# Performance work log

Measured on AMD Instinct MI355X. Metric: run time of the kernel, lower is better.

Reference implementation:

```python
import jax, jax.numpy as jnp
import numpy as np
from jax import lax

SEQ_LEN = 8192
N_FEATURES = 1
E = 128            # embedding_dim
H1 = 2 * E         # 256
H2 = 4 * E         # 512


def _lstm_params(key, in_dim, hidden):
    k1, k2, k3, k4 = jax.random.split(key, 4)
    s = 1.0 / np.sqrt(hidden)
    return (
        jax.random.uniform(k1, (4 * hidden, in_dim), jnp.float32, -s, s),   # Wih
        jax.random.uniform(k2, (4 * hidden, hidden), jnp.float32, -s, s),   # Whh
        jax.random.uniform(k3, (4 * hidden,), jnp.float32, -s, s),          # bih
        jax.random.uniform(k4, (4 * hidden,), jnp.float32, -s, s),          # bhh
    )


def lstm(x, Wih, Whh, bih, bhh):
    """Single-layer PyTorch-convention LSTM over x:[T,in]. Returns (ys:[T,H], h_T:[H])."""
    H = Whh.shape[1]
    # precompute input contribution for all timesteps (memory-bound GEMM once)
    xg = x @ Wih.T + (bih + bhh)  # [T, 4H]

    def step(carry, gx):
        h, c = carry
        g = gx + h @ Whh.T
        i, f, gc, o = jnp.split(g, 4)
        i = jax.nn.sigmoid(i)
        f = jax.nn.sigmoid(f)
        gc = jnp.tanh(gc)
        o = jax.nn.sigmoid(o)
        c = f * c + i * gc
        h = o * jnp.tanh(c)
        return (h, c), h

    init = (jnp.zeros((H,), x.dtype), jnp.zeros((H,), x.dtype))
    (hT, _), ys = lax.scan(step, init, xg)
    return ys, hT


def setup_inputs() -> dict:
    key = jax.random.key(0)
    keys = jax.random.split(key, 8)
    inp = {"x": jax.random.normal(keys[0], (SEQ_LEN, N_FEATURES), jnp.float32)}
    # encoder: n_features -> H2 -> H1 -> E
    for name, k, din, dh in [("e1", keys[1], N_FEATURES, H2), ("e2", keys[2], H2, H1), ("e3", keys[3], H1, E),
                             ("d1", keys[4], E, E), ("d2", keys[5], E, H1), ("d3", keys[6], H1, H2)]:
        Wih, Whh, bih, bhh = _lstm_params(k, din, dh)
        inp[name + "_Wih"], inp[name + "_Whh"], inp[name + "_bih"], inp[name + "_bhh"] = Wih, Whh, bih, bhh
    ko1, ko2 = jax.random.split(keys[7])
    s = 1.0 / np.sqrt(H2)
    inp["out_W"] = jax.random.uniform(ko1, (N_FEATURES, H2), jnp.float32, -s, s)
    inp["out_b"] = jax.random.uniform(ko2, (N_FEATURES,), jnp.float32, -s, s)
    return inp


def reference(x,
              e1_Wih, e1_Whh, e1_bih, e1_bhh,
              e2_Wih, e2_Whh, e2_bih, e2_bhh,
              e3_Wih, e3_Whh, e3_bih, e3_bhh,
              d1_Wih, d1_Whh, d1_bih, d1_bhh,
              d2_Wih, d2_Whh, d2_bih, d2_bhh,
              d3_Wih, d3_Whh, d3_bih, d3_bhh,
              out_W, out_b):
    # --- encoder ---
    xs = x.reshape(SEQ_LEN, N_FEATURES)
    ys, _ = lstm(xs, e1_Wih, e1_Whh, e1_bih, e1_bhh)   # [T, H2]
    ys, _ = lstm(ys, e2_Wih, e2_Whh, e2_bih, e2_bhh)   # [T, H1]
    _, hT = lstm(ys, e3_Wih, e3_Whh, e3_bih, e3_bhh)   # hT: [E]
    z = hT.reshape(N_FEATURES, E)                       # [1, E]
    # --- decoder: repeat latent across time ---
    zr = jnp.tile(z.reshape(1, E), (SEQ_LEN, 1))        # [T, E]
    ys, _ = lstm(zr, d1_Wih, d1_Whh, d1_bih, d1_bhh)    # [T, E]
    ys, _ = lstm(ys, d2_Wih, d2_Whh, d2_bih, d2_bhh)    # [T, H1]
    ys, _ = lstm(ys, d3_Wih, d3_Whh, d3_bih, d3_bhh)    # [T, H2]
    return ys @ out_W.T + out_b                          # [T, 1]
```

## Files before the change

kernel.cpp:

```cpp
#include <hip/hip_runtime.h>
#include <stdint.h>

#define T_LEN 8192

__device__ __forceinline__ float sigf(float x) {
    return 1.0f / (1.0f + __expf(-x));
}
__device__ __forceinline__ float tanh_fast(float x) {
    float e = __expf(2.0f * x);
    return 1.0f - 2.0f / (e + 1.0f);
}

template<int H, int NWG, int TPB, int SUBS, int XGMODE, int LID, bool WRITE_YS, bool WRITE_Z>
__global__ __launch_bounds__(TPB, TPB / 256)
void lstm_scan(const float* __restrict__ Whh,
               const float* __restrict__ xg,
               const float* __restrict__ wih0,
               const float* __restrict__ bih,
               const float* __restrict__ bhh,
               float* __restrict__ ys,
               unsigned long long* __restrict__ hst,
               float* __restrict__ zout)
{
    constexpr int ROWS = 4 * H / NWG;
    constexpr int HJ   = H / NWG;
    constexpr int CH   = H / SUBS;
    constexpr int CHP  = CH + 4;
    static_assert(ROWS * SUBS == TPB, "bad layout");
    static_assert(4 * SUBS <= 64, "gate group must fit a wave");

    const int tid = threadIdx.x;
    const int wg  = (NWG > 1) ? blockIdx.x : 0;
    const int q   = tid / SUBS;
    const int sub = tid % SUBS;
    const int jj  = q >> 2;
    const int g   = q & 3;
    const int grow = g * H + wg * HJ + jj;

    __shared__ float hbuf[2 * SUBS * CHP];
    __shared__ float xsh[XGMODE == 1 ? T_LEN : 1];
    __shared__ int abortf;

    float4 wreg[CH / 4];
    {
        const float4* wr = (const float4*)(Whh + (size_t)grow * H + sub * CH);
        #pragma unroll
        for (int i = 0; i < CH / 4; ++i) wreg[i] = wr[i];
    }

    float w0 = 0.f, bs = 0.f, xgc = 0.f;
    if constexpr (XGMODE == 1) { w0 = wih0[grow]; bs = bih[grow] + bhh[grow]; }
    if constexpr (XGMODE == 2) { xgc = xg[grow]; }
    if constexpr (XGMODE == 1) {
        for (int k = tid; k < T_LEN; k += TPB) xsh[k] = xg[k];
    }

    for (int k = tid; k < 2 * SUBS * CHP; k += TPB) hbuf[k] = 0.f;
    if (tid == 0) abortf = 0;

    const bool writer = (tid % (4 * SUBS)) == 0;
    const int  wjj    = tid / (4 * SUBS);
    float c = 0.f;

    float xgv = 0.f;
    if constexpr (XGMODE == 0) { if (sub == 0) xgv = xg[grow]; }

    for (int t = 0; t < T_LEN; ++t) {
        float xgn = 0.f;
        if constexpr (XGMODE == 0) {
            if (sub == 0 && t + 1 < T_LEN) xgn = xg[(size_t)(t + 1) * (4 * H) + grow];
        }

        if constexpr (NWG > 1) {
            if (t > 0 && tid < H && (tid / HJ) != wg) {
                const size_t idx = (size_t)(t - 1) * H + tid;
                const unsigned want = (unsigned)(LID * T_LEN + t);
                unsigned long long v;
                int spin = 0;
                for (;;) {
                    v = __hip_atomic_load(&hst[idx], __ATOMIC_RELAXED,
                                          __HIP_MEMORY_SCOPE_AGENT);
                    if ((unsigned)(v >> 32) == want) break;
                    if (++spin >= (1 << 22)) { abortf = 1; break; }
                }
                union { unsigned u; float f; } cv;
                cv.u = (unsigned)v;
                hbuf[(t & 1) * SUBS * CHP + (tid / CH) * CHP + (tid % CH)] = cv.f;
            }
        }
        __syncthreads();
        if constexpr (NWG > 1) { if (abortf) break; }

        const float* hb = &hbuf[(t & 1) * SUBS * CHP + sub * CHP];
        float4 a4 = make_float4(0.f, 0.f, 0.f, 0.f);
        #pragma unroll
        for (int i = 0; i < CH / 4; ++i) {
            float4 hv = *(const float4*)&hb[i * 4];
            float4 wv = wreg[i];
            a4.x = fmaf(wv.x, hv.x, a4.x);
            a4.y = fmaf(wv.y, hv.y, a4.y);
            a4.z = fmaf(wv.z, hv.z, a4.z);
            a4.w = fmaf(wv.w, hv.w, a4.w);
        }
        float acc = (a4.x + a4.y) + (a4.z + a4.w);
        #pragma unroll
        for (int d = 1; d < SUBS; d <<= 1) acc += __shfl_xor(acc, d);

        float base;
        if constexpr (XGMODE == 0)      base = xgv;
        else if constexpr (XGMODE == 1) base = fmaf(xsh[t], w0, bs);
        else                            base = xgc;
        float gv = acc + base;
        float av = (g == 2) ? tanh_fast(gv) : sigf(gv);

        float fv = __shfl_down(av, SUBS);
        float gc = __shfl_down(av, 2 * SUBS);
        float ov = __shfl_down(av, 3 * SUBS);

        if (writer) {
            c = fmaf(fv, c, av * gc);
            float h = ov * tanh_fast(c);
            const int e = wg * HJ + wjj;
            hbuf[((t + 1) & 1) * SUBS * CHP + (e / CH) * CHP + (e % CH)] = h;
            if constexpr (WRITE_YS) ys[(size_t)t * H + e] = h;
            if constexpr (NWG > 1) {
                union { float f; unsigned u; } cv;
                cv.f = h;
                unsigned long long pk =
                    ((unsigned long long)(unsigned)(LID * T_LEN + t + 1) << 32) | cv.u;
                __hip_atomic_store(&hst[(size_t)t * H + e], pk,
                                   __ATOMIC_RELAXED, __HIP_MEMORY_SCOPE_AGENT);
            }
            if constexpr (WRITE_Z) { if (t == T_LEN - 1) zout[e] = h; }
        }
        if constexpr (XGMODE == 0) xgv = xgn;
    }
}

__global__ __launch_bounds__(256)
void gemm_bias(const float* __restrict__ A, const float* __restrict__ B,
               const float* __restrict__ bih, const float* __restrict__ bhh,
               float* __restrict__ C, int M, int N, int K)
{
    __shared__ float As[16][72];
    __shared__ float Bs[16][72];
    const int tid = threadIdx.x;
    const int bm = blockIdx.y * 64;
    const int bn = blockIdx.x * 64;
    const int tm = (tid / 16) * 4;
    const int tn = (tid % 16) * 4;
    const int lr = tid >> 2;
    const int lc = (tid & 3) * 4;
    float acc[4][4] = {{0.f}};
    for (int k0 = 0; k0 < K; k0 += 16) {
        float4 va = *(const float4*)&A[(size_t)(bm + lr) * K + k0 + lc];
        float4 vb = *(const float4*)&B[(size_t)(bn + lr) * K + k0 + lc];
        As[lc + 0][lr] = va.x; As[lc + 1][lr] = va.y;
        As[lc + 2][lr] = va.z; As[lc + 3][lr] = va.w;
        Bs[lc + 0][lr] = vb.x; Bs[lc + 1][lr] = vb.y;
        Bs[lc + 2][lr] = vb.z; Bs[lc + 3][lr] = vb.w;
        __syncthreads();
        #pragma unroll
        for (int kk = 0; kk < 16; ++kk) {
            float4 av = *(const float4*)&As[kk][tm];
            float4 bv = *(const float4*)&Bs[kk][tn];
            float ar[4] = {av.x, av.y, av.z, av.w};
            float br[4] = {bv.x, bv.y, bv.z, bv.w};
            #pragma unroll
            for (int i = 0; i < 4; ++i)
                #pragma unroll
                for (int j = 0; j < 4; ++j)
                    acc[i][j] = fmaf(ar[i], br[j], acc[i][j]);
        }
        __syncthreads();
    }
    float bsum[4];
    #pragma unroll
    for (int j = 0; j < 4; ++j) bsum[j] = bih[bn + tn + j] + bhh[bn + tn + j];
    #pragma unroll
    for (int i = 0; i < 4; ++i) {
        float4 o;
        o.x = acc[i][0] + bsum[0];
        o.y = acc[i][1] + bsum[1];
        o.z = acc[i][2] + bsum[2];
        o.w = acc[i][3] + bsum[3];
        *(float4*)&C[(size_t)(bm + tm + i) * N + bn + tn] = o;
    }
}

__global__ __launch_bounds__(512)
void xg_const_d1(const float* __restrict__ z, const float* __restrict__ Wih,
                 const float* __restrict__ bih, const float* __restrict__ bhh,
                 float* __restrict__ xgd1)
{
    __shared__ float zs[128];
    const int tid = threadIdx.x;
    if (tid < 128) zs[tid] = z[tid];
    __syncthreads();
    const float4* wr = (const float4*)(Wih + (size_t)tid * 128);
    float4 a4 = make_float4(0.f, 0.f, 0.f, 0.f);
    #pragma unroll
    for (int i = 0; i < 32; ++i) {
        float4 w = wr[i];
        float4 h = *(const float4*)&zs[i * 4];
        a4.x = fmaf(w.x, h.x, a4.x); a4.y = fmaf(w.y, h.y, a4.y);
        a4.z = fmaf(w.z, h.z, a4.z); a4.w = fmaf(w.w, h.w, a4.w);
    }
    xgd1[tid] = (a4.x + a4.y) + (a4.z + a4.w) + bih[tid] + bhh[tid];
}

__global__ __launch_bounds__(256)
void out_gemv(const float* __restrict__ ys, const float* __restrict__ Wo,
              const float* __restrict__ bo, float* __restrict__ out)
{
    const int lane = threadIdx.x & 63;
    const int wid  = threadIdx.x >> 6;
    const int t = blockIdx.x * 4 + wid;
    const float* row = ys + (size_t)t * 512;
    float a = 0.f;
    #pragma unroll
    for (int i = 0; i < 8; ++i) a = fmaf(row[lane + i * 64], Wo[lane + i * 64], a);
    #pragma unroll
    for (int d = 1; d < 64; d <<= 1) a += __shfl_xor(a, d);
    if (lane == 0) out[t] = a + bo[0];
}

template<int H, int NWG, int TPB, int SUBS, int XGMODE, int LID, bool YS, bool Z>
static void launch_scan(const float* whh, const float* xg, const float* wih0,
                        const float* bih, const float* bhh, float* ys,
                        unsigned long long* hst, float* zout, hipStream_t stream)
{
    auto kfn = lstm_scan<H, NWG, TPB, SUBS, XGMODE, LID, YS, Z>;
    if (NWG > 1) {
        void* args[8] = {&whh, &xg, &wih0, &bih, &bhh, &ys, &hst, &zout};
        hipError_t e = hipLaunchCooperativeKernel(reinterpret_cast<void*>(kfn),
                                                  dim3(NWG), dim3(TPB), args, 0u, stream);
        if (e == hipSuccess) return;
    }
    kfn<<<dim3(NWG), dim3(TPB), 0, stream>>>(whh, xg, wih0, bih, bhh, ys, hst, zout);
}

extern "C" void kernel_launch(void* const* d_in, const int* in_sizes, int n_in,
                              void* d_out, int out_size, void* d_ws, size_t ws_size,
                              hipStream_t stream)
{
    (void)in_sizes; (void)n_in; (void)out_size;
    const float* x = (const float*)d_in[0];
    const float* Wih[6]; const float* Whh[6]; const float* Bih[6]; const float* Bhh[6];
    for (int l = 0; l < 6; ++l) {
        Wih[l] = (const float*)d_in[1 + l * 4 + 0];
        Whh[l] = (const float*)d_in[1 + l * 4 + 1];
        Bih[l] = (const float*)d_in[1 + l * 4 + 2];
        Bhh[l] = (const float*)d_in[1 + l * 4 + 3];
    }
    const float* outW = (const float*)d_in[25];
    const float* outb = (const float*)d_in[26];

    char* ws = (char*)d_ws;
    float* XG  = (float*)(ws);
    float* ysA = (float*)(ws + ((size_t)64 << 20));
    float* ysB = (float*)(ws + ((size_t)80 << 20));
    unsigned long long* HST = (unsigned long long*)(ws + ((size_t)96 << 20));
    float* z    = (float*)(ws + ((size_t)128 << 20));
    float* xgd1 = (float*)(ws + ((size_t)128 << 20) + 1024);
    if (ws_size < (((size_t)128 << 20) + 4096)) return;

    launch_scan<512, 32, 512, 8, 1, 1, true, false>(Whh[0], x, Wih[0], Bih[0], Bhh[0],
                                                    ysA, HST, nullptr, stream);
    gemm_bias<<<dim3(1024 / 64, T_LEN / 64), 256, 0, stream>>>(ysA, Wih[1], Bih[1], Bhh[1],
                                                               XG, T_LEN, 1024, 512);
    launch_scan<256, 16, 512, 8, 0, 2, true, false>(Whh[1], XG, nullptr, nullptr, nullptr,
                                                    ysB, HST, nullptr, stream);
    gemm_bias<<<dim3(512 / 64, T_LEN / 64), 256, 0, stream>>>(ysB, Wih[2], Bih[2], Bhh[2],
                                                              XG, T_LEN, 512, 256);
    launch_scan<128, 1, 512, 1, 0, 0, false, true>(Whh[2], XG, nullptr, nullptr, nullptr,
                                                   nullptr, nullptr, z, stream);

    xg_const_d1<<<1, 512, 0, stream>>>(z, Wih[3], Bih[3], Bhh[3], xgd1);
    launch_scan<128, 1, 512, 1, 2, 0, true, false>(Whh[3], xgd1, nullptr, nullptr, nullptr,
                                                   ysA, nullptr, nullptr, stream);
    gemm_bias<<<dim3(1024 / 64, T_LEN / 64), 256, 0, stream>>>(ysA, Wih[4], Bih[4], Bhh[4],
                                                               XG, T_LEN, 1024, 128);
    launch_scan<256, 16, 512, 8, 0, 3, true, false>(Whh[4], XG, nullptr, nullptr, nullptr,
                                                    ysB, HST, nullptr, stream);
    gemm_bias<<<dim3(2048 / 64, T_LEN / 64), 256, 0, stream>>>(ysB, Wih[5], Bih[5], Bhh[5],
                                                               XG, T_LEN, 2048, 256);
    launch_scan<512, 32, 512, 8, 0, 4, true, false>(Whh[5], XG, nullptr, nullptr, nullptr,
                                                    ysA, HST, nullptr, stream);

    out_gemv<<<dim3(T_LEN / 4), 256, 0, stream>>>(ysA, outW, outb, (float*)d_out);
}
```

Before: 71.00 ms.

## Stage recurrent weights in LDS and split H=128 scans across workgroups

Each scan workgroup now copies its slice of the recurrent weights into padded shared memory and reads them from there every step, instead of holding them in registers. The input-scalar path for the first layer no longer stages the whole sequence in shared memory; it prefetches the next input value from global memory each step. The two 128-wide layers (last encoder, first decoder) now run across 4 cooperating workgroups that exchange hidden state through global memory each step, rather than in one workgroup. Sequence IDs are renumbered so the per-step exchange tags stay unique. This cuts register pressure and the serial dot length per thread, but adds shared-memory weight traffic and cross-workgroup synchronisation latency on every timestep.

```diff
diff --git a/kernel.cpp b/kernel.cpp
--- a/kernel.cpp
+++ b/kernel.cpp
@@ -26,6 +26,7 @@
     constexpr int HJ   = H / NWG;
     constexpr int CH   = H / SUBS;
     constexpr int CHP  = CH + 4;
+    constexpr int WST  = H + 4;
     static_assert(ROWS * SUBS == TPB, "bad layout");
     static_assert(4 * SUBS <= 64, "gate group must fit a wave");
 
@@ -37,26 +38,32 @@
     const int g   = q & 3;
     const int grow = g * H + wg * HJ + jj;
 
+    __shared__ float WL[ROWS * WST];
     __shared__ float hbuf[2 * SUBS * CHP];
-    __shared__ float xsh[XGMODE == 1 ? T_LEN : 1];
+    __shared__ float w0s[XGMODE == 1 ? ROWS : 1];
+    __shared__ float bss[XGMODE == 1 ? ROWS : 1];
     __shared__ int abortf;
 
-    float4 wreg[CH / 4];
-    {
-        const float4* wr = (const float4*)(Whh + (size_t)grow * H + sub * CH);
-        #pragma unroll
-        for (int i = 0; i < CH / 4; ++i) wreg[i] = wr[i];
-    }
-
-    float w0 = 0.f, bs = 0.f, xgc = 0.f;
-    if constexpr (XGMODE == 1) { w0 = wih0[grow]; bs = bih[grow] + bhh[grow]; }
+    for (int idx = tid; idx < ROWS * H / 4; idx += TPB) {
+        const int rq = idx / (H / 4);
+        const int c4 = idx % (H / 4);
+        const int gr = (rq & 3) * H + wg * HJ + (rq >> 2);
+        float4 v = *(const float4*)&Whh[(size_t)gr * H + c4 * 4];
+        *(float4*)&WL[rq * WST + c4 * 4] = v;
+    }
+    if constexpr (XGMODE == 1) {
+        for (int rq = tid; rq < ROWS; rq += TPB) {
+            const int gr = (rq & 3) * H + wg * HJ + (rq >> 2);
+            w0s[rq] = wih0[gr];
+            bss[rq] = bih[gr] + bhh[gr];
+        }
+    }
+    float xgc = 0.f;
     if constexpr (XGMODE == 2) { xgc = xg[grow]; }
-    if constexpr (XGMODE == 1) {
-        for (int k = tid; k < T_LEN; k += TPB) xsh[k] = xg[k];
-    }
 
     for (int k = tid; k < 2 * SUBS * CHP; k += TPB) hbuf[k] = 0.f;
     if (tid == 0) abortf = 0;
+    __syncthreads();
 
     const bool writer = (tid % (4 * SUBS)) == 0;
     const int  wjj    = tid / (4 * SUBS);
@@ -64,11 +71,18 @@
 
     float xgv = 0.f;
     if constexpr (XGMODE == 0) { if (sub == 0) xgv = xg[grow]; }
+    float xcur = 0.f;
+    if constexpr (XGMODE == 1) { xcur = xg[0]; }
+
+    const float* wrow = &WL[q * WST + sub * CH];
 
     for (int t = 0; t < T_LEN; ++t) {
-        float xgn = 0.f;
+        float xgn = 0.f, xnext = 0.f;
         if constexpr (XGMODE == 0) {
             if (sub == 0 && t + 1 < T_LEN) xgn = xg[(size_t)(t + 1) * (4 * H) + grow];
+        }
+        if constexpr (XGMODE == 1) {
+            if (t + 1 < T_LEN) xnext = xg[t + 1];
         }
 
         if constexpr (NWG > 1) {
@@ -96,7 +110,7 @@
         #pragma unroll
         for (int i = 0; i < CH / 4; ++i) {
             float4 hv = *(const float4*)&hb[i * 4];
-            float4 wv = wreg[i];
+            float4 wv = *(const float4*)&wrow[i * 4];
             a4.x = fmaf(wv.x, hv.x, a4.x);
             a4.y = fmaf(wv.y, hv.y, a4.y);
             a4.z = fmaf(wv.z, hv.z, a4.z);
@@ -108,7 +122,7 @@
 
         float base;
         if constexpr (XGMODE == 0)      base = xgv;
-        else if constexpr (XGMODE == 1) base = fmaf(xsh[t], w0, bs);
+        else if constexpr (XGMODE == 1) base = fmaf(xcur, w0s[q], bss[q]);
         else                            base = xgc;
         float gv = acc + base;
         float av = (g == 2) ? tanh_fast(gv) : sigf(gv);
@@ -134,6 +148,7 @@
             if constexpr (WRITE_Z) { if (t == T_LEN - 1) zout[e] = h; }
         }
         if constexpr (XGMODE == 0) xgv = xgn;
+        if constexpr (XGMODE == 1) xcur = xnext;
     }
 }
 
@@ -273,19 +288,19 @@
                                                     ysB, HST, nullptr, stream);
     gemm_bias<<<dim3(512 / 64, T_LEN / 64), 256, 0, stream>>>(ysB, Wih[2], Bih[2], Bhh[2],
                                                               XG, T_LEN, 512, 256);
-    launch_scan<128, 1, 512, 1, 0, 0, false, true>(Whh[2], XG, nullptr, nullptr, nullptr,
-                                                   nullptr, nullptr, z, stream);
+    launch_scan<128, 4, 512, 4, 0, 3, false, true>(Whh[2], XG, nullptr, nullptr, nullptr,
+                                                   nullptr, HST, z, stream);
 
     xg_const_d1<<<1, 512, 0, stream>>>(z, Wih[3], Bih[3], Bhh[3], xgd1);
-    launch_scan<128, 1, 512, 1, 2, 0, true, false>(Whh[3], xgd1, nullptr, nullptr, nullptr,
-                                                   ysA, nullptr, nullptr, stream);
+    launch_scan<128, 4, 512, 4, 2, 4, true, false>(Whh[3], xgd1, nullptr, nullptr, nullptr,
+                                                   ysA, HST, nullptr, stream);
     gemm_bias<<<dim3(1024 / 64, T_LEN / 64), 256, 0, stream>>>(ysA, Wih[4], Bih[4], Bhh[4],
                                                                XG, T_LEN, 1024, 128);
-    launch_scan<256, 16, 512, 8, 0, 3, true, false>(Whh[4], XG, nullptr, nullptr, nullptr,
+    launch_scan<256, 16, 512, 8, 0, 5, true, false>(Whh[4], XG, nullptr, nullptr, nullptr,
                                                     ysB, HST, nullptr, stream);
     gemm_bias<<<dim3(2048 / 64, T_LEN / 64), 256, 0, stream>>>(ysB, Wih[5], Bih[5], Bhh[5],
                                                                XG, T_LEN, 2048, 256);
-    launch_scan<512, 32, 512, 8, 0, 4, true, false>(Whh[5], XG, nullptr, nullptr, nullptr,
+    launch_scan<512, 32, 512, 8, 0, 6, true, false>(Whh[5], XG, nullptr, nullptr, nullptr,
                                                     ysA, HST, nullptr, stream);
 
     out_gemv<<<dim3(T_LEN / 4), 256, 0, stream>>>(ysA, outW, outb, (float*)d_out);
```

After: 94.26 ms. +32.8%, slower.
